# Performance work log

Measured on AMD Instinct MI355X. Metric: run time of the kernel, lower is better.

The kernel has to match this reference:

```python
import jax, jax.numpy as jnp
import numpy as np

ALPHA = 0.2          # LeakyReLU negative slope
NEG = -9e15          # mask fill value, as in pyGAT GraphAttentionLayer
N, NIN, NHID, NOUT = 4096, 64, 32, 64
NHEADS, D_INT = 8, 32
H_INT = max(1, int(NHEADS * 0.25))   # 2 intent heads
H_SP = NHEADS - H_INT                # 6 spatial heads


def setup_inputs() -> dict:
    key = jax.random.key(0)
    ks = jax.random.split(key, 10)
    x = jax.random.normal(ks[0], (N, NIN), dtype=jnp.float32)
    adj = (jax.random.uniform(ks[1], (N, N)) < 0.01).astype(jnp.float32)
    adj = jnp.clip(adj + jnp.eye(N, dtype=jnp.float32), 0.0, 1.0)
    intent_embeds = jax.random.normal(ks[2], (N, D_INT), dtype=jnp.float32)
    # learned params (xavier-ish scale)
    def xav(k, shape):
        fan = shape[-2] if len(shape) > 1 else shape[-1]
        return jax.random.normal(k, shape, dtype=jnp.float32) / np.sqrt(fan)
    W_sp = xav(ks[3], (H_SP, NIN, NHID))       # spatial head projections
    a_sp = xav(ks[4], (H_SP, 2 * NHID))        # spatial attention vectors
    W_int = xav(ks[5], (H_INT, NIN, NHID))     # intent head projections
    a_int = xav(ks[6], (H_INT, 2 * D_INT))     # intent attention vectors (over intent embeds)
    W_out = xav(ks[7], (NHID * NHEADS, NOUT))  # output GAT layer
    a_out = xav(ks[8], (2 * NOUT,))
    return {"x": x, "adj": adj, "intent_embeds": intent_embeds,
            "W_sp": W_sp, "a_sp": a_sp, "W_int": W_int, "a_int": a_int,
            "W_out": W_out, "a_out": a_out}


def _masked_attend(e, mask, Wh):
    # e: [H,N,N] raw scores, mask: [1,N,N] bool, Wh: [H,N,F]
    att = jax.nn.softmax(jnp.where(mask, e, NEG), axis=-1)
    return jnp.einsum('hij,hjf->hif', att, Wh)


def reference(x, adj, intent_embeds, W_sp, a_sp, W_int, a_int, W_out, a_out):
    mask = (adj > 0)[None]                                   # [1,N,N]
    # ---- spatial heads (standard GAT, batched over heads) ----
    Wh_s = jnp.einsum('nf,hfo->hno', x, W_sp)                # [Hs,N,nhid]
    f1 = jnp.einsum('hno,ho->hn', Wh_s, a_sp[:, :NHID])
    f2 = jnp.einsum('hno,ho->hn', Wh_s, a_sp[:, NHID:])
    e_s = jax.nn.leaky_relu(f1[:, :, None] + f2[:, None, :], ALPHA)
    h_s = jax.nn.elu(_masked_attend(e_s, mask, Wh_s))        # concat=True -> elu
    # ---- intent heads: scores from intent embeddings, values from Wh ----
    Wh_i = jnp.einsum('nf,hfo->hno', x, W_int)               # [Hi,N,nhid]
    g1 = jnp.einsum('nd,hd->hn', intent_embeds, a_int[:, :D_INT])
    g2 = jnp.einsum('nd,hd->hn', intent_embeds, a_int[:, D_INT:])
    e_i = jax.nn.leaky_relu(g1[:, :, None] + g2[:, None, :], ALPHA)
    h_i = jax.nn.elu(_masked_attend(e_i, mask, Wh_i))        # [Hi,N,nhid]
    # ---- concat heads along feature dim: [N, nheads*nhid] ----
    h = jnp.concatenate([h_s, h_i], axis=0).transpose(1, 0, 2).reshape(N, -1)
    # ---- output attention layer (concat=False: no elu) ----
    Who = h @ W_out                                          # [N,nout]
    o1 = Who @ a_out[:NOUT]
    o2 = Who @ a_out[NOUT:]
    e_o = jax.nn.leaky_relu(o1[:, None] + o2[None, :], ALPHA)
    att_o = jax.nn.softmax(jnp.where(mask[0], e_o, NEG), axis=-1)
    out = att_o @ Who
    return jnp.tanh(out)
```

## Files before the change

kernel.cpp:

```cpp
#include <hip/hip_runtime.h>

#define N      4096
#define NIN    64
#define NHID   32
#define NOUT   64
#define NHEADS 8
#define H_SP   6
#define D_INT  32
#define MAXDEG 128
#define WCAP   80
#define ALPHA  0.2f

typedef float vf4 __attribute__((ext_vector_type(4)));

__global__ __launch_bounds__(256) void k_fused1(
    const float* __restrict__ x, const float* __restrict__ ie,
    const vf4* __restrict__ adj4,
    const float* __restrict__ Wsp, const float* __restrict__ asp,
    const float* __restrict__ Wint, const float* __restrict__ aint,
    float* __restrict__ Wh_t, float* __restrict__ src, float* __restrict__ dst_t,
    int* __restrict__ col, int* __restrict__ deg)
{
    const int n    = blockIdx.x;
    const int tid  = threadIdx.x;
    const int wv   = tid >> 6, lane = tid & 63;
    const int h    = tid >> 5, f    = tid & 31;

    __shared__ float xs[NIN];
    __shared__ float ies[D_INT];
    __shared__ int   wbuf[4][WCAP];
    __shared__ int   wcnt[4];

    const vf4* row = adj4 + (size_t)n * (N / 4) + wv * 256 + lane;
    vf4 a0 = __builtin_nontemporal_load(row);
    vf4 a1 = __builtin_nontemporal_load(row + 64);
    vf4 a2 = __builtin_nontemporal_load(row + 128);
    vf4 a3 = __builtin_nontemporal_load(row + 192);

    if (tid < NIN) xs[tid] = x[n * NIN + tid];
    else if (tid < NIN + D_INT) ies[tid - NIN] = ie[n * D_INT + (tid - NIN)];
    __syncthreads();

    const float* W = (h < H_SP) ? (Wsp + h * NIN * NHID)
                                : (Wint + (h - H_SP) * NIN * NHID);
    float acc0 = 0.f, acc1 = 0.f;
#pragma unroll
    for (int c = 0; c < NIN; c += 2) {
        acc0 += xs[c]     * W[c * NHID + f];
        acc1 += xs[c + 1] * W[(c + 1) * NHID + f];
    }
    const float acc = acc0 + acc1;
    Wh_t[(size_t)n * 256 + tid] = acc;

    float s1, s2;
    if (h < H_SP) {
        s1 = acc * asp[h * 2 * NHID + f];
        s2 = acc * asp[h * 2 * NHID + NHID + f];
    } else {
        float v = ies[f];
        s1 = v * aint[(h - H_SP) * 2 * D_INT + f];
        s2 = v * aint[(h - H_SP) * 2 * D_INT + D_INT + f];
    }
#pragma unroll
    for (int m = 16; m >= 1; m >>= 1) {
        s1 += __shfl_xor(s1, m);
        s2 += __shfl_xor(s2, m);
    }
    if (f == 0) { src[h * N + n] = s1; dst_t[n * 8 + h] = s2; }

    int cnt = 0;
#pragma unroll
    for (int t = 0; t < 4; ++t) {
        vf4 v = (t == 0) ? a0 : (t == 1) ? a1 : (t == 2) ? a2 : a3;
        unsigned nib = (v.x > 0.f ? 1u : 0u) | (v.y > 0.f ? 2u : 0u)
                     | (v.z > 0.f ? 4u : 0u) | (v.w > 0.f ? 8u : 0u);
        int c = __popc(nib);
        int scan = c;
#pragma unroll
        for (int m = 1; m <= 32; m <<= 1) {
            int o = __shfl_up(scan, m);
            if (lane >= m) scan += o;
        }
        int pos = cnt + scan - c;
        int idx0 = (wv * 256 + t * 64 + lane) * 4;
        if (nib) {
            if (nib & 1u) { if (pos < WCAP) wbuf[wv][pos] = idx0;     ++pos; }
            if (nib & 2u) { if (pos < WCAP) wbuf[wv][pos] = idx0 + 1; ++pos; }
            if (nib & 4u) { if (pos < WCAP) wbuf[wv][pos] = idx0 + 2; ++pos; }
            if (nib & 8u) { if (pos < WCAP) wbuf[wv][pos] = idx0 + 3; ++pos; }
        }
        cnt += __shfl(scan, 63);
    }
    if (lane == 0) wcnt[wv] = cnt;
    __syncthreads();

    const int c0 = wcnt[0], c1 = wcnt[1], c2 = wcnt[2], c3 = wcnt[3];
    const int off = (wv > 0 ? c0 : 0) + (wv > 1 ? c1 : 0) + (wv > 2 ? c2 : 0);
    const int my = (wcnt[wv] < WCAP) ? wcnt[wv] : WCAP;
    for (int i = lane; i < my; i += 64) {
        int p = off + i;
        if (p < MAXDEG) col[n * MAXDEG + p] = wbuf[wv][i];
    }
    if (tid == 0) {
        int tot = c0 + c1 + c2 + c3;
        deg[n] = (tot < MAXDEG) ? tot : MAXDEG;
    }
}

__global__ __launch_bounds__(256) void k_attn1who(
    const int* __restrict__ col, const int* __restrict__ deg,
    const float* __restrict__ Wh_t, const float* __restrict__ src,
    const float* __restrict__ dst_t, const float* __restrict__ Wout,
    const float* __restrict__ aout,
    float* __restrict__ Who, float* __restrict__ o1, float* __restrict__ o2)
{
    const int r   = blockIdx.x;
    const int tid = threadIdx.x;
    const int h   = tid >> 5, lane = tid & 31;

    __shared__ int   cs[MAXDEG];
    __shared__ float w[NHEADS][MAXDEG];
    __shared__ float hs[NHEADS * NHID];
    __shared__ float part[4][NOUT];

    const int d  = deg[r];
    const int d8 = (d + 7) & ~7;
    for (int k = tid; k < MAXDEG; k += 256)
        cs[k] = (k < d) ? col[r * MAXDEG + k] : 0;
    __syncthreads();

    const float sr = src[h * N + r];
    float ev[4];
    float mx = -3.4e38f;
#pragma unroll
    for (int t = 0; t < 4; ++t) {
        int k = lane + t * 32;
        float e = -3.4e38f;
        if (k < d) {
            e = sr + dst_t[cs[k] * 8 + h];
            e = e > 0.f ? e : ALPHA * e;
        }
        ev[t] = e;
        mx = fmaxf(mx, e);
    }
#pragma unroll
    for (int m = 16; m >= 1; m >>= 1) mx = fmaxf(mx, __shfl_xor(mx, m));

    float sum = 0.f;
#pragma unroll
    for (int t = 0; t < 4; ++t) {
        int k = lane + t * 32;
        float p = (k < d) ? __expf(ev[t] - mx) : 0.f;
        ev[t] = p;
        sum += p;
    }
#pragma unroll
    for (int m = 16; m >= 1; m >>= 1) sum += __shfl_xor(sum, m);
    const float inv = 1.f / sum;

#pragma unroll
    for (int t = 0; t < 4; ++t) {
        int k = lane + t * 32;
        w[h][k] = (k < d) ? ev[t] * inv : 0.f;
    }
    __syncthreads();

    float acc0 = 0.f, acc1 = 0.f;
    for (int k = 0; k < d8; k += 8) {
        int4   ja = *(const int4*)  &cs[k];
        int4   jb = *(const int4*)  &cs[k + 4];
        float4 wa = *(const float4*)&w[h][k];
        float4 wb = *(const float4*)&w[h][k + 4];
        float g0 = Wh_t[(size_t)ja.x * 256 + tid];
        float g1 = Wh_t[(size_t)ja.y * 256 + tid];
        float g2 = Wh_t[(size_t)ja.z * 256 + tid];
        float g3 = Wh_t[(size_t)ja.w * 256 + tid];
        float g4 = Wh_t[(size_t)jb.x * 256 + tid];
        float g5 = Wh_t[(size_t)jb.y * 256 + tid];
        float g6 = Wh_t[(size_t)jb.z * 256 + tid];
        float g7 = Wh_t[(size_t)jb.w * 256 + tid];
        acc0 += wa.x * g0 + wa.y * g1 + wa.z * g2 + wa.w * g3;
        acc1 += wb.x * g4 + wb.y * g5 + wb.z * g6 + wb.w * g7;
    }
    float acc = acc0 + acc1;
    acc = acc > 0.f ? acc : __expf(acc) - 1.f;
    hs[tid] = acc;
    __syncthreads();

    const int fo = tid & 63, q = tid >> 6;
    float p = 0.f;
#pragma unroll
    for (int c = q * 64; c < q * 64 + 64; ++c) p += hs[c] * Wout[c * NOUT + fo];
    part[q][fo] = p;
    __syncthreads();

    if (tid < 64) {
        float who = part[0][tid] + part[1][tid] + part[2][tid] + part[3][tid];
        Who[(size_t)r * NOUT + tid] = who;
        float v1 = who * aout[tid];
        float v2 = who * aout[NOUT + tid];
#pragma unroll
        for (int m = 32; m >= 1; m >>= 1) {
            v1 += __shfl_xor(v1, m);
            v2 += __shfl_xor(v2, m);
        }
        if (tid == 0) { o1[r] = v1; o2[r] = v2; }
    }
}

__global__ __launch_bounds__(256) void k_attn2(
    const int* __restrict__ col, const int* __restrict__ deg,
    const float* __restrict__ Who, const float* __restrict__ o1,
    const float* __restrict__ o2, float* __restrict__ out)
{
    const int r   = blockIdx.x;
    const int tid = threadIdx.x;
    const int wv  = tid >> 6, lane = tid & 63;

    __shared__ int   cs[MAXDEG];
    __shared__ float w[MAXDEG];
    __shared__ float part[4][NOUT];
    __shared__ float redm[4], reds[4];

    const int d = deg[r];
    for (int k = tid; k < MAXDEG; k += 256)
        cs[k] = (k < d) ? col[r * MAXDEG + k] : 0;
    __syncthreads();

    const float sr = o1[r];
    float e = -3.4e38f;
    if (tid < d) {
        e = sr + o2[cs[tid]];
        e = e > 0.f ? e : ALPHA * e;
    }
    float mx = e;
#pragma unroll
    for (int m = 32; m >= 1; m >>= 1) mx = fmaxf(mx, __shfl_xor(mx, m));
    if (lane == 0) redm[wv] = mx;
    __syncthreads();
    mx = fmaxf(fmaxf(redm[0], redm[1]), fmaxf(redm[2], redm[3]));

    float p = (tid < d) ? __expf(e - mx) : 0.f;
    float s = p;
#pragma unroll
    for (int m = 32; m >= 1; m >>= 1) s += __shfl_xor(s, m);
    if (lane == 0) reds[wv] = s;
    __syncthreads();
    const float inv = 1.f / (reds[0] + reds[1] + reds[2] + reds[3]);
    if (tid < MAXDEG) w[tid] = p * inv;
    __syncthreads();

    const int kup = (d + 31) & ~31;
    float acc0 = 0.f, acc1 = 0.f;
    for (int k = wv * 8; k < kup; k += 32) {
        int4   ja = *(const int4*)  &cs[k];
        int4   jb = *(const int4*)  &cs[k + 4];
        float4 wa = *(const float4*)&w[k];
        float4 wb = *(const float4*)&w[k + 4];
        acc0 += wa.x * Who[(size_t)ja.x * NOUT + lane];
        acc0 += wa.y * Who[(size_t)ja.y * NOUT + lane];
        acc0 += wa.z * Who[(size_t)ja.z * NOUT + lane];
        acc0 += wa.w * Who[(size_t)ja.w * NOUT + lane];
        acc1 += wb.x * Who[(size_t)jb.x * NOUT + lane];
        acc1 += wb.y * Who[(size_t)jb.y * NOUT + lane];
        acc1 += wb.z * Who[(size_t)jb.z * NOUT + lane];
        acc1 += wb.w * Who[(size_t)jb.w * NOUT + lane];
    }
    part[wv][lane] = acc0 + acc1;
    __syncthreads();

    if (tid < NOUT)
        out[(size_t)r * NOUT + tid] =
            tanhf(part[0][tid] + part[1][tid] + part[2][tid] + part[3][tid]);
}

extern "C" void kernel_launch(void* const* d_in, const int* in_sizes, int n_in,
                              void* d_out, int out_size, void* d_ws, size_t ws_size,
                              hipStream_t stream) {
    const float* x    = (const float*)d_in[0];
    const float* adj  = (const float*)d_in[1];
    const float* ie   = (const float*)d_in[2];
    const float* Wsp  = (const float*)d_in[3];
    const float* asp  = (const float*)d_in[4];
    const float* Wint = (const float*)d_in[5];
    const float* aint = (const float*)d_in[6];
    const float* Wout = (const float*)d_in[7];
    const float* aout = (const float*)d_in[8];
    float* out = (float*)d_out;

    float* ws    = (float*)d_ws;
    float* Wh_t  = ws;
    float* src   = Wh_t + 1048576;
    float* dst_t = src  + 32768;
    float* Who   = dst_t + 32768;
    float* o1    = Who  + 262144;
    float* o2    = o1   + 4096;
    int*   col   = (int*)(o2 + 4096);
    int*   deg   = col + 4096 * MAXDEG;

    k_fused1  <<<N, 256, 0, stream>>>(x, ie, (const vf4*)adj, Wsp, asp,
                                      Wint, aint, Wh_t, src, dst_t, col, deg);
    k_attn1who<<<N, 256, 0, stream>>>(col, deg, Wh_t, src, dst_t, Wout, aout,
                                      Who, o1, o2);
    k_attn2   <<<N, 256, 0, stream>>>(col, deg, Who, o1, o2, out);
}
```

Before: 162.2 us.

## Process four nodes per block in fused projection and per-wave adjacency compaction

The first kernel now handles four nodes per block. Each W weight load is reused across four rows of x, and each wave scans one full adjacency row by itself, writing column indices straight to global memory. This removes the shared-memory staging buffer, the second block barrier and the cross-wave offset merge, and launches a quarter as many blocks. In exchange, each wave issues 16 serial loads per row without nontemporal hints, which lowers memory-level parallelism per row and may expose load latency on the 64 MB adjacency scan.

```diff
diff --git a/kernel.cpp b/kernel.cpp
--- a/kernel.cpp
+++ b/kernel.cpp
@@ -8,70 +8,62 @@
 #define H_SP   6
 #define D_INT  32
 #define MAXDEG 128
-#define WCAP   80
+#define NPB    4
 #define ALPHA  0.2f
-
-typedef float vf4 __attribute__((ext_vector_type(4)));
 
 __global__ __launch_bounds__(256) void k_fused1(
     const float* __restrict__ x, const float* __restrict__ ie,
-    const vf4* __restrict__ adj4,
+    const float4* __restrict__ adj4,
     const float* __restrict__ Wsp, const float* __restrict__ asp,
     const float* __restrict__ Wint, const float* __restrict__ aint,
     float* __restrict__ Wh_t, float* __restrict__ src, float* __restrict__ dst_t,
     int* __restrict__ col, int* __restrict__ deg)
 {
-    const int n    = blockIdx.x;
+    const int nb   = blockIdx.x * NPB;
     const int tid  = threadIdx.x;
     const int wv   = tid >> 6, lane = tid & 63;
     const int h    = tid >> 5, f    = tid & 31;
 
-    __shared__ float xs[NIN];
-    __shared__ float ies[D_INT];
-    __shared__ int   wbuf[4][WCAP];
-    __shared__ int   wcnt[4];
-
-    const vf4* row = adj4 + (size_t)n * (N / 4) + wv * 256 + lane;
-    vf4 a0 = __builtin_nontemporal_load(row);
-    vf4 a1 = __builtin_nontemporal_load(row + 64);
-    vf4 a2 = __builtin_nontemporal_load(row + 128);
-    vf4 a3 = __builtin_nontemporal_load(row + 192);
-
-    if (tid < NIN) xs[tid] = x[n * NIN + tid];
-    else if (tid < NIN + D_INT) ies[tid - NIN] = ie[n * D_INT + (tid - NIN)];
+    __shared__ float xs[NPB][NIN];
+    __shared__ float ies[NPB][D_INT];
+
+    xs[tid >> 6][tid & 63] = x[nb * NIN + tid];
+    if (tid < NPB * D_INT) ies[tid >> 5][tid & 31] = ie[nb * D_INT + tid];
     __syncthreads();
 
     const float* W = (h < H_SP) ? (Wsp + h * NIN * NHID)
                                 : (Wint + (h - H_SP) * NIN * NHID);
-    float acc0 = 0.f, acc1 = 0.f;
-#pragma unroll
-    for (int c = 0; c < NIN; c += 2) {
-        acc0 += xs[c]     * W[c * NHID + f];
-        acc1 += xs[c + 1] * W[(c + 1) * NHID + f];
-    }
-    const float acc = acc0 + acc1;
-    Wh_t[(size_t)n * 256 + tid] = acc;
-
-    float s1, s2;
-    if (h < H_SP) {
-        s1 = acc * asp[h * 2 * NHID + f];
-        s2 = acc * asp[h * 2 * NHID + NHID + f];
-    } else {
-        float v = ies[f];
-        s1 = v * aint[(h - H_SP) * 2 * D_INT + f];
-        s2 = v * aint[(h - H_SP) * 2 * D_INT + D_INT + f];
-    }
-#pragma unroll
-    for (int m = 16; m >= 1; m >>= 1) {
-        s1 += __shfl_xor(s1, m);
-        s2 += __shfl_xor(s2, m);
-    }
-    if (f == 0) { src[h * N + n] = s1; dst_t[n * 8 + h] = s2; }
-
+    float acc[NPB] = {0.f, 0.f, 0.f, 0.f};
+#pragma unroll
+    for (int c = 0; c < NIN; ++c) {
+        const float wval = W[c * NHID + f];
+#pragma unroll
+        for (int m = 0; m < NPB; ++m) acc[m] += xs[m][c] * wval;
+    }
+#pragma unroll
+    for (int m = 0; m < NPB; ++m)
+        Wh_t[(size_t)(nb + m) * 256 + tid] = acc[m];
+
+    const float a1v = (h < H_SP) ? asp[h * 64 + f]      : aint[(h - H_SP) * 64 + f];
+    const float a2v = (h < H_SP) ? asp[h * 64 + 32 + f] : aint[(h - H_SP) * 64 + 32 + f];
+#pragma unroll
+    for (int m = 0; m < NPB; ++m) {
+        const float b = (h < H_SP) ? acc[m] : ies[m][f];
+        float s1 = b * a1v, s2 = b * a2v;
+#pragma unroll
+        for (int mm = 16; mm >= 1; mm >>= 1) {
+            s1 += __shfl_xor(s1, mm);
+            s2 += __shfl_xor(s2, mm);
+        }
+        if (f == 0) { src[h * N + nb + m] = s1; dst_t[(nb + m) * 8 + h] = s2; }
+    }
+
+    const int r = nb + wv;
+    const float4* row = adj4 + (size_t)r * (N / 4);
     int cnt = 0;
-#pragma unroll
-    for (int t = 0; t < 4; ++t) {
-        vf4 v = (t == 0) ? a0 : (t == 1) ? a1 : (t == 2) ? a2 : a3;
+#pragma unroll 4
+    for (int t = 0; t < 16; ++t) {
+        float4 v = row[t * 64 + lane];
         unsigned nib = (v.x > 0.f ? 1u : 0u) | (v.y > 0.f ? 2u : 0u)
                      | (v.z > 0.f ? 4u : 0u) | (v.w > 0.f ? 8u : 0u);
         int c = __popc(nib);
@@ -82,29 +74,16 @@
             if (lane >= m) scan += o;
         }
         int pos = cnt + scan - c;
-        int idx0 = (wv * 256 + t * 64 + lane) * 4;
+        int idx0 = (t * 64 + lane) * 4;
         if (nib) {
-            if (nib & 1u) { if (pos < WCAP) wbuf[wv][pos] = idx0;     ++pos; }
-            if (nib & 2u) { if (pos < WCAP) wbuf[wv][pos] = idx0 + 1; ++pos; }
-            if (nib & 4u) { if (pos < WCAP) wbuf[wv][pos] = idx0 + 2; ++pos; }
-            if (nib & 8u) { if (pos < WCAP) wbuf[wv][pos] = idx0 + 3; ++pos; }
+            if (nib & 1u) { if (pos < MAXDEG) col[r * MAXDEG + pos] = idx0;     ++pos; }
+            if (nib & 2u) { if (pos < MAXDEG) col[r * MAXDEG + pos] = idx0 + 1; ++pos; }
+            if (nib & 4u) { if (pos < MAXDEG) col[r * MAXDEG + pos] = idx0 + 2; ++pos; }
+            if (nib & 8u) { if (pos < MAXDEG) col[r * MAXDEG + pos] = idx0 + 3; ++pos; }
         }
         cnt += __shfl(scan, 63);
     }
-    if (lane == 0) wcnt[wv] = cnt;
-    __syncthreads();
-
-    const int c0 = wcnt[0], c1 = wcnt[1], c2 = wcnt[2], c3 = wcnt[3];
-    const int off = (wv > 0 ? c0 : 0) + (wv > 1 ? c1 : 0) + (wv > 2 ? c2 : 0);
-    const int my = (wcnt[wv] < WCAP) ? wcnt[wv] : WCAP;
-    for (int i = lane; i < my; i += 64) {
-        int p = off + i;
-        if (p < MAXDEG) col[n * MAXDEG + p] = wbuf[wv][i];
-    }
-    if (tid == 0) {
-        int tot = c0 + c1 + c2 + c3;
-        deg[n] = (tot < MAXDEG) ? tot : MAXDEG;
-    }
+    if (lane == 0) deg[r] = (cnt < MAXDEG) ? cnt : MAXDEG;
 }
 
 __global__ __launch_bounds__(256) void k_attn1who(
@@ -298,9 +277,9 @@
     int*   col   = (int*)(o2 + 4096);
     int*   deg   = col + 4096 * MAXDEG;
 
-    k_fused1  <<<N, 256, 0, stream>>>(x, ie, (const vf4*)adj, Wsp, asp,
-                                      Wint, aint, Wh_t, src, dst_t, col, deg);
-    k_attn1who<<<N, 256, 0, stream>>>(col, deg, Wh_t, src, dst_t, Wout, aout,
-                                      Who, o1, o2);
-    k_attn2   <<<N, 256, 0, stream>>>(col, deg, Who, o1, o2, out);
-}
+    k_fused1  <<<N / NPB, 256, 0, stream>>>(x, ie, (const float4*)adj, Wsp, asp,
+                                            Wint, aint, Wh_t, src, dst_t, col, deg);
+    k_attn1who<<<N,       256, 0, stream>>>(col, deg, Wh_t, src, dst_t, Wout, aout,
+                                            Who, o1, o2);
+    k_attn2   <<<N,       256, 0, stream>>>(col, deg, Who, o1, o2, out);
+}
```

Result: faster. 156.7 us (-3.4%).
